# Performance work log

Measured on AMD Instinct MI355X. Metric: run time of the kernel, lower is better.

## Reference

```python
import jax, jax.numpy as jnp
import numpy as np

K_MASK = -2.3819763e+38
NUM_HEADS = 16
NUM_KV_HEADS = 8
HEAD_DIM = 128
FEATURES = 2048
QUERY_SCALE = 0.08838834764831845  # head_dim ** -0.5
ROPE_BASE = 10000
SOFT_CAP = 50.0
WINDOW = 1024


def apply_rope(inputs, positions, base_frequency=ROPE_BASE):
    # inputs: [B, L, N, H], positions: [B, L]
    head_dim = inputs.shape[-1]
    fraction = 2.0 * jnp.arange(0, head_dim // 2, dtype=jnp.float32) / head_dim
    timescale = jnp.asarray(base_frequency, jnp.float32) ** fraction
    sinusoid = positions[..., None].astype(jnp.float32) / timescale[None, None, :]
    sinusoid = sinusoid[..., None, :]  # [B, L, 1, H/2]
    sin, cos = jnp.sin(sinusoid), jnp.cos(sinusoid)
    first, second = jnp.split(inputs, 2, axis=-1)
    out = jnp.concatenate([first * cos - second * sin,
                           second * cos + first * sin], axis=-1)
    return out.astype(inputs.dtype)


def setup_inputs() -> dict:
    key = jax.random.key(0)
    ks = jax.random.split(key, 4)
    B, T, D = 2, 2048, FEATURES
    x = jax.random.normal(ks[0], (B, T, D), dtype=jnp.float32)
    segment_pos = jnp.broadcast_to(jnp.arange(T, dtype=jnp.int32)[None, :], (B, T))
    # causal prefill mask [B, T, S] with S == T
    attn_mask = jnp.broadcast_to(
        jnp.tril(jnp.ones((T, T), dtype=bool))[None], (B, T, T))
    wq = jax.random.normal(ks[1], (NUM_HEADS, D, HEAD_DIM), dtype=jnp.float32) * 0.02
    wkv = jax.random.normal(ks[2], (2, NUM_KV_HEADS, D, HEAD_DIM), dtype=jnp.float32) * 0.02
    wo = jax.random.normal(ks[3], (NUM_HEADS, HEAD_DIM, D), dtype=jnp.float32) * 0.02
    return {"x": x, "segment_pos": segment_pos, "attn_mask": attn_mask,
            "wq": wq, "wkv": wkv, "wo": wo}


def reference(x, segment_pos, attn_mask, wq, wkv, wo):
    # Projections
    q = jnp.einsum('BTD,NDH->BTNH', x, wq)              # [B,T,N,H]
    kv = jnp.einsum('BSD,CKDH->CBSKH', x, wkv)          # [2,B,S,K,H]
    k, v = kv[0], kv[1]

    # RoPE + query scaling
    q = apply_rope(q, segment_pos) * QUERY_SCALE
    k = apply_rope(k, segment_pos)

    # GQA: fold query heads into (K groups, G heads per group)
    B, T, N, H = q.shape
    K, G = NUM_KV_HEADS, N // NUM_KV_HEADS
    qg = q.reshape(B, T, K, G, H)
    logits = jnp.einsum('BTKGH,BSKH->BTKGS', qg, k).reshape(B, T, N, -1)

    # Logit soft-capping
    logits = jnp.tanh(logits / SOFT_CAP) * SOFT_CAP

    # Sliding-window mask (prefill: end_index=0, cache_len = S)
    S = attn_mask.shape[-1]
    cache_positions = jnp.arange(S)[None, None, :]       # [1,1,S]
    sp = segment_pos[:, :, None]                         # [B,T,1]
    sliding = (cache_positions > sp - WINDOW) & (cache_positions < sp + WINDOW)
    mask = jnp.logical_and(attn_mask, sliding)

    padded = jnp.where(mask[:, :, None, :], logits, K_MASK)
    probs = jax.nn.softmax(padded, axis=-1).astype(k.dtype)

    pg = probs.reshape(B, T, K, G, S)
    encoded = jnp.einsum('BTKGS,BSKH->BTKGH', pg, v).reshape(B, T, N, H)
    return jnp.einsum('BTNH,NHD->BTD', encoded, wo)
```

## Files before the change

kernel.cpp:

```cpp
#include <hip/hip_runtime.h>

typedef __attribute__((ext_vector_type(8))) short short8;
typedef __attribute__((ext_vector_type(4))) float f32x4;
typedef __attribute__((ext_vector_type(4))) float f4;
typedef __attribute__((ext_vector_type(4))) unsigned short u16x4;

__device__ __forceinline__ unsigned short f2bf(float f) {
    union { float f; unsigned int u; } v; v.f = f;
    unsigned int r = v.u + 0x7fffu + ((v.u >> 16) & 1u);
    return (unsigned short)(r >> 16);
}
__device__ __forceinline__ float bf2f(unsigned short h) {
    union { unsigned int u; float f; } v; v.u = ((unsigned int)h) << 16;
    return v.f;
}
__device__ __forceinline__ void gload_lds16(const void* g, void* l) {
    __builtin_amdgcn_global_load_lds(
        (const __attribute__((address_space(1))) unsigned int*)g,
        (__attribute__((address_space(3))) unsigned int*)l, 16, 0, 0);
}


__global__ void conv_x(const float* __restrict__ x, unsigned short* __restrict__ xb) {
    int i = blockIdx.x * 256 + threadIdx.x;
    f4 v = ((const f4*)x)[i];
    u16x4 o;
    o[0] = f2bf(v[0]); o[1] = f2bf(v[1]); o[2] = f2bf(v[2]); o[3] = f2bf(v[3]);
    ((u16x4*)xb)[i] = o;
}

__global__ void conv_wqkvt(const float* __restrict__ wq, const float* __restrict__ wkv,
                           unsigned short* __restrict__ wt) {
    __shared__ float tile[64 * 65];
    const int d0 = blockIdx.x * 64, f0 = blockIdx.y * 64;
    const int head = f0 >> 7;
    const int h0 = f0 & 127;
    const float* src;
    float scl;
    if (head < 16) { src = wq + (size_t)head * 2048 * 128; scl = 0.08838834764831845f; }
    else           { src = wkv + (size_t)(head - 16) * 2048 * 128; scl = 1.f; }
    {
        int hh = threadIdx.x & 63, dq = threadIdx.x >> 6;
        #pragma unroll
        for (int r = 0; r < 16; ++r) {
            int dd = r * 4 + dq;
            tile[dd * 65 + hh] = src[(size_t)(d0 + dd) * 128 + h0 + hh] * scl;
        }
    }
    __syncthreads();
    {
        int dd = threadIdx.x & 63, fq = threadIdx.x >> 6;
        #pragma unroll
        for (int r = 0; r < 16; ++r) {
            int fl = r * 4 + fq;
            wt[(size_t)(f0 + fl) * 2048 + d0 + dd] = f2bf(tile[dd * 65 + fl]);
        }
    }
}

__global__ void conv_wot(const float* __restrict__ wo, unsigned short* __restrict__ wt) {
    __shared__ float tile[64 * 65];
    const int d0 = blockIdx.x * 64, r0 = blockIdx.y * 64;
    int cc = threadIdx.x & 63, rq = threadIdx.x >> 6;
    #pragma unroll
    for (int r = 0; r < 16; ++r) {
        int rr = r * 4 + rq;
        tile[rr * 65 + cc] = wo[(size_t)(r0 + rr) * 2048 + d0 + cc];
    }
    __syncthreads();
    #pragma unroll
    for (int r = 0; r < 16; ++r) {
        int rr = r * 4 + rq;
        wt[(size_t)(d0 + rr) * 2048 + r0 + cc] = f2bf(tile[cc * 65 + rr]);
    }
}


__global__ __launch_bounds__(512, 2)
void gemm8p(const unsigned short* __restrict__ A,
            const unsigned short* __restrict__ Bt,
            unsigned short* __restrict__ C,
            int ldk, int ldc, int nt, int ksplit, size_t cstride) {
    __shared__ __align__(16) unsigned short LDS[65536];
    const int tid = threadIdx.x, lane = tid & 63, w = tid >> 6;
    const int wr = w >> 2, wc = w & 3;
    const int l15 = lane & 15, l4 = lane >> 4;
    int nwg = gridDim.x * gridDim.y;
    int wg = blockIdx.y * gridDim.x + blockIdx.x;
    int swz = (wg & 7) * (nwg >> 3) + (wg >> 3);
    int bx = swz % gridDim.x, by = swz / gridDim.x;
    int slice = 0;
    if (ksplit) { slice = by & 1; by >>= 1; }
    unsigned short* Cs = C + (size_t)slice * cstride;
    const int brow = by * 256, bcol = bx * 256;
    const size_t koff = (size_t)slice * nt * 64;
    const int wg_a = w & 3;
    const int wg_b = wr;
    const int rA = wg_a * 8 + (lane >> 3);
    const int rB = wg_b * 8 + (lane >> 3);
    const int cgS = ((lane & 7) ^ (lane >> 3)) * 8;
    const unsigned short* aP = A + (size_t)(brow + wr * 128 + rA) * ldk + koff + cgS;
    const unsigned short* bP = Bt + (size_t)(bcol + wc * 64 + rB) * ldk + koff + cgS;
    const int ldsA0 = wr * 8192 + (wg_a * 64 + lane) * 8;
    const int ldsB0 = wc * 4096 + (wg_b * 64 + lane) * 8;
    const int aRd = (wr * 128 + l15) * 64;
    const int bRd = (wc * 64 + l15) * 64;
    const int c0 = ((0 + l4) ^ (l15 & 7)) * 8;
    const int c1 = ((4 + l4) ^ (l15 & 7)) * 8;
    f32x4 acc[8][4] = {};
    gload_lds16(aP,                    &LDS[ldsA0]);
    gload_lds16(bP,                    &LDS[16384 + ldsB0]);
    gload_lds16(aP + (size_t)32 * ldk, &LDS[ldsA0 + 2048]);
    gload_lds16(bP + (size_t)16 * ldk, &LDS[16384 + ldsB0 + 1024]);
    gload_lds16(bP + (size_t)32 * ldk, &LDS[16384 + ldsB0 + 2048]);
    gload_lds16(bP + (size_t)48 * ldk, &LDS[16384 + ldsB0 + 3072]);
    gload_lds16(aP + (size_t)64 * ldk, &LDS[ldsA0 + 4096]);
    gload_lds16(aP + (size_t)96 * ldk, &LDS[ldsA0 + 6144]);
    asm volatile("s_waitcnt vmcnt(4)" ::: "memory");
    __builtin_amdgcn_s_barrier();
    __builtin_amdgcn_sched_barrier(0);

    short8 af[4][2], bl[2][2], bh[2][2];
    for (int t = 0; t < nt; ++t) {
        const int bufA = (t & 1) << 15, bufB = bufA + 16384;
        const bool pf = (t + 1) < nt;
        const int sA = ((t + 1) & 1) << 15, sB = sA + 16384;
        const unsigned short* ap = aP + (t + 1) * 64;
        const unsigned short* bp = bP + (t + 1) * 64;
        #pragma unroll
        for (int m = 0; m < 4; ++m) {
            af[m][0] = *(const short8*)&LDS[bufA + aRd + m * 1024 + c0];
            af[m][1] = *(const short8*)&LDS[bufA + aRd + m * 1024 + c1];
        }
        #pragma unroll
        for (int n = 0; n < 2; ++n) {
            bl[n][0] = *(const short8*)&LDS[bufB + bRd + n * 1024 + c0];
            bl[n][1] = *(const short8*)&LDS[bufB + bRd + n * 1024 + c1];
        }
        if (pf) { gload_lds16(ap, &LDS[sA + ldsA0]);
                  gload_lds16(bp, &LDS[sB + ldsB0]); }
        __builtin_amdgcn_s_barrier();
        __builtin_amdgcn_sched_barrier(0);
        __builtin_amdgcn_s_setprio(1);
        #pragma unroll
        for (int kk = 0; kk < 2; ++kk)
            #pragma unroll
            for (int m = 0; m < 4; ++m)
                #pragma unroll
                for (int n = 0; n < 2; ++n)
                    acc[m][n] = __builtin_amdgcn_mfma_f32_16x16x32_bf16(af[m][kk], bl[n][kk], acc[m][n], 0, 0, 0);
        __builtin_amdgcn_s_setprio(0);
        asm volatile("s_waitcnt vmcnt(4)" ::: "memory");
        __builtin_amdgcn_s_barrier();
        __builtin_amdgcn_sched_barrier(0);
        #pragma unroll
        for (int n = 0; n < 2; ++n) {
            bh[n][0] = *(const short8*)&LDS[bufB + bRd + (n + 2) * 1024 + c0];
            bh[n][1] = *(const short8*)&LDS[bufB + bRd + (n + 2) * 1024 + c1];
        }
        if (pf) { gload_lds16(ap + (size_t)32 * ldk, &LDS[sA + ldsA0 + 2048]);
                  gload_lds16(bp + (size_t)16 * ldk, &LDS[sB + ldsB0 + 1024]); }
        __builtin_amdgcn_s_barrier();
        __builtin_amdgcn_sched_barrier(0);
        __builtin_amdgcn_s_setprio(1);
        #pragma unroll
        for (int kk = 0; kk < 2; ++kk)
            #pragma unroll
            for (int m = 0; m < 4; ++m)
                #pragma unroll
                for (int n = 0; n < 2; ++n)
                    acc[m][n + 2] = __builtin_amdgcn_mfma_f32_16x16x32_bf16(af[m][kk], bh[n][kk], acc[m][n + 2], 0, 0, 0);
        __builtin_amdgcn_s_setprio(0);
        asm volatile("s_waitcnt vmcnt(4)" ::: "memory");
        __builtin_amdgcn_s_barrier();
        __builtin_amdgcn_sched_barrier(0);
        #pragma unroll
        for (int m = 0; m < 4; ++m) {
            af[m][0] = *(const short8*)&LDS[bufA + aRd + (m + 4) * 1024 + c0];
            af[m][1] = *(const short8*)&LDS[bufA + aRd + (m + 4) * 1024 + c1];
        }
        if (pf) { gload_lds16(bp + (size_t)32 * ldk, &LDS[sB + ldsB0 + 2048]);
                  gload_lds16(bp + (size_t)48 * ldk, &LDS[sB + ldsB0 + 3072]); }
        __builtin_amdgcn_s_barrier();
        __builtin_amdgcn_sched_barrier(0);
        __builtin_amdgcn_s_setprio(1);
        #pragma unroll
        for (int kk = 0; kk < 2; ++kk)
            #pragma unroll
            for (int m = 0; m < 4; ++m)
                #pragma unroll
                for (int n = 0; n < 2; ++n)
                    acc[m + 4][n] = __builtin_amdgcn_mfma_f32_16x16x32_bf16(af[m][kk], bl[n][kk], acc[m + 4][n], 0, 0, 0);
        __builtin_amdgcn_s_setprio(0);
        __builtin_amdgcn_s_barrier();
        __builtin_amdgcn_sched_barrier(0);
        if (pf) { gload_lds16(ap + (size_t)64 * ldk, &LDS[sA + ldsA0 + 4096]);
                  gload_lds16(ap + (size_t)96 * ldk, &LDS[sA + ldsA0 + 6144]); }
        __builtin_amdgcn_s_barrier();
        __builtin_amdgcn_sched_barrier(0);
        __builtin_amdgcn_s_setprio(1);
        #pragma unroll
        for (int kk = 0; kk < 2; ++kk)
            #pragma unroll
            for (int m = 0; m < 4; ++m)
                #pragma unroll
                for (int n = 0; n < 2; ++n)
                    acc[m + 4][n + 2] = __builtin_amdgcn_mfma_f32_16x16x32_bf16(af[m][kk], bh[n][kk], acc[m + 4][n + 2], 0, 0, 0);
        __builtin_amdgcn_s_setprio(0);
        asm volatile("s_waitcnt vmcnt(4)" ::: "memory");
        __builtin_amdgcn_s_barrier();
        __builtin_amdgcn_sched_barrier(0);
    }
    #pragma unroll
    for (int m = 0; m < 8; ++m)
        #pragma unroll
        for (int n = 0; n < 4; ++n)
            #pragma unroll
            for (int j = 0; j < 4; ++j) {
                int row = brow + wr * 128 + m * 16 + l4 * 4 + j;
                int col = bcol + wc * 64 + n * 16 + l15;
                Cs[(size_t)row * ldc + col] = f2bf(acc[m][n][j]);
            }
}

__global__ void addparts(const unsigned short* __restrict__ p0,
                         const unsigned short* __restrict__ p1,
                         float* __restrict__ out) {
    int i = blockIdx.x * 256 + threadIdx.x;
    short8 a = ((const short8*)p0)[i];
    short8 b = ((const short8*)p1)[i];
    f4 lo, hi;
    #pragma unroll
    for (int j = 0; j < 4; ++j)
        lo[j] = bf2f((unsigned short)a[j]) + bf2f((unsigned short)b[j]);
    #pragma unroll
    for (int j = 0; j < 4; ++j)
        hi[j] = bf2f((unsigned short)a[j + 4]) + bf2f((unsigned short)b[j + 4]);
    ((f4*)out)[2 * i] = lo;
    ((f4*)out)[2 * i + 1] = hi;
}

__global__ void rope_reshape(const unsigned short* __restrict__ qkv,
                             const int* __restrict__ segpos,
                             unsigned short* __restrict__ q_r,
                             unsigned short* __restrict__ k_r) {
    const int bt = blockIdx.x;
    const int hd = blockIdx.y * 2 + (threadIdx.x >> 7);
    const int b = bt >> 11, t = bt & 2047;
    const int h = threadIdx.x & 127;
    const unsigned short* in = (hd < 16)
        ? qkv + (size_t)bt * 4096 + hd * 128
        : qkv + (size_t)bt * 4096 + 2048 + (hd - 16) * 128;
    int pos = segpos[bt];
    int i = h & 63;
    float inv_ts = __expf((float)i * (-9.210340371976184f / 64.f));
    float ang = (float)pos * inv_ts;
    float s = __sinf(ang), c = __cosf(ang);
    float x1 = bf2f(in[i]);
    float x2 = bf2f(in[i + 64]);
    float o = (h < 64) ? (x1 * c - x2 * s) : (x2 * c + x1 * s);
    if (hd < 16) {
        q_r[((size_t)((b * 16 + hd) * 2048 + t)) * 128 + h] = f2bf(o);
    } else {
        int kh = hd - 16;
        k_r[((size_t)((b * 8 + kh) * 2048 + t)) * 128 + h] = f2bf(o);
    }
}

__global__ void v_transpose(const unsigned short* __restrict__ qkv,
                            unsigned short* __restrict__ v_t) {
    __shared__ unsigned short tile[64][72];
    const int tt0 = blockIdx.x * 64;
    const int kh = blockIdx.y >> 1, hb = (blockIdx.y & 1) * 64;
    const int b = blockIdx.z;
    int c = threadIdx.x & 63, rq = threadIdx.x >> 6;
    #pragma unroll
    for (int r = 0; r < 16; ++r) {
        int tt = r * 4 + rq;
        tile[tt][c] = qkv[(size_t)(b * 2048 + tt0 + tt) * 4096 + 3072 + kh * 128 + hb + c];
    }
    __syncthreads();
    #pragma unroll
    for (int r = 0; r < 16; ++r) {
        int hr = r * 4 + rq;
        v_t[((size_t)(b * 8 + kh) * 128 + hb + hr) * 2048 + tt0 + c] = tile[c][hr];
    }
}


__device__ __forceinline__ void stage_kv(const unsigned short* kbase, const unsigned short* vbase,
                                         unsigned short* Ksb, unsigned short* Vtb,
                                         int st, int tid) {
    #pragma unroll
    for (int r = 0; r < 2; ++r) {
        int e = (r * 512 + tid) * 8;
        int krow = e >> 7, kcol = e & 127;
        gload_lds16(kbase + (size_t)(st * 64 + krow) * 128 + (kcol ^ ((krow & 7) << 3)), Ksb + e);
        int vrow = e >> 6, vcol = e & 63;
        gload_lds16(vbase + (size_t)vrow * 2048 + st * 64 + (vcol ^ ((vrow & 7) << 3)), Vtb + e);
    }
}

__global__ __launch_bounds__(512, 4)
void attn_kernel(const unsigned short* __restrict__ q_r,
                 const unsigned short* __restrict__ k_r,
                 const unsigned short* __restrict__ v_t,
                 unsigned short* __restrict__ enc) {
    __shared__ __align__(16) unsigned short Ks[2][64 * 128];
    __shared__ __align__(16) unsigned short Vt[2][128 * 64];
    __shared__ __align__(16) unsigned short Pl[8][16 * 64];
    const int tid = threadIdx.x, lane = tid & 63, wave = tid >> 6;
    const int l15 = lane & 15, l4 = lane >> 4;
    const int flat = blockIdx.x;
    const int xcd = flat & 7, g = flat >> 3;
    const int pair = xcd * 2 + (g >> 5);
    const int qb = 31 - (g & 31);
    const int kh = pair >> 1, b = pair & 1;
    const int n = kh * 2 + (wave >> 2);
    const int wq = wave & 3;
    short8 qf[4];
    {
        const unsigned short* qp =
            q_r + ((size_t)((b * 16 + n) * 2048 + qb * 64 + wq * 16 + l15)) * 128 + l4 * 8;
        #pragma unroll
        for (int kk = 0; kk < 4; ++kk) qf[kk] = *(const short8*)(qp + kk * 32);
    }
    f32x4 Of[8] = {};
    float lrow[4] = {};
    int t_lo = qb * 64 - 1023; if (t_lo < 0) t_lo = 0;
    const int st0 = t_lo >> 6;
    const unsigned short* kbase = k_r + (size_t)(b * 8 + kh) * 2048 * 128;
    const unsigned short* vbase = v_t + (size_t)(b * 8 + kh) * 128 * 2048;

    stage_kv(kbase, vbase, Ks[0], Vt[0], st0, tid);
    __syncthreads();
    int cur = 0;
    for (int st = st0; st <= qb; ++st) {
        if (st < qb)
            stage_kv(kbase, vbase, Ks[cur ^ 1], Vt[cur ^ 1], st + 1, tid);
        f32x4 sf[4] = {};
        #pragma unroll
        for (int nc = 0; nc < 4; ++nc) {
            int row = nc * 16 + l15;
            int sw = (l15 & 7) << 3;
            #pragma unroll
            for (int kk = 0; kk < 4; ++kk) {
                short8 bfr = *(const short8*)&Ks[cur][row * 128 + ((kk * 32 + l4 * 8) ^ sw)];
                sf[nc] = __builtin_amdgcn_mfma_f32_16x16x32_bf16(qf[kk], bfr, sf[nc], 0, 0, 0);
            }
        }
        const int mode = (st == qb) ? 1 : ((qb >= 16 && st == st0) ? 2 : 0);
        #pragma unroll
        for (int j = 0; j < 4; ++j) {
            int trow = qb * 64 + wq * 16 + l4 * 4 + j;
            int prow = l4 * 4 + j;
            int psw = (prow & 7) << 3;
            #pragma unroll
            for (int nc = 0; nc < 4; ++nc) {
                float ex = __expf(sf[nc][j] * 0.04f);
                float p = __expf(-100.f * __builtin_amdgcn_rcpf(ex + 1.f));
                if (mode) {
                    int s = st * 64 + nc * 16 + l15;
                    bool ok = (mode == 1) ? (s <= trow) : (s >= trow - 1023);
                    p = ok ? p : 0.f;
                }
                lrow[j] += p;
                Pl[wave][prow * 64 + ((nc * 16 + l15) ^ psw)] = f2bf(p);
            }
        }
        {
            int asw = (l15 & 7) << 3;
            #pragma unroll
            for (int ks = 0; ks < 2; ++ks) {
                short8 af = *(const short8*)&Pl[wave][l15 * 64 + ((ks * 32 + l4 * 8) ^ asw)];
                #pragma unroll
                for (int hc = 0; hc < 8; ++hc) {
                    int vrow = hc * 16 + l15;
                    short8 bfr = *(const short8*)&Vt[cur][vrow * 64 + ((ks * 32 + l4 * 8) ^ asw)];
                    Of[hc] = __builtin_amdgcn_mfma_f32_16x16x32_bf16(af, bfr, Of[hc], 0, 0, 0);
                }
            }
        }
        __syncthreads();
        cur ^= 1;
    }
    float inv[4];
    #pragma unroll
    for (int j = 0; j < 4; ++j) {
        float l = lrow[j];
        l += __shfl_xor(l, 1); l += __shfl_xor(l, 2);
        l += __shfl_xor(l, 4); l += __shfl_xor(l, 8);
        inv[j] = 1.f / l;
    }
    #pragma unroll
    for (int hc = 0; hc < 8; ++hc)
        #pragma unroll
        for (int j = 0; j < 4; ++j) {
            size_t row = (size_t)(b * 2048 + qb * 64 + wq * 16 + l4 * 4 + j);
            enc[row * 2048 + n * 128 + hc * 16 + l15] = f2bf(Of[hc][j] * inv[j]);
        }
}


extern "C" void kernel_launch(void* const* d_in, const int* in_sizes, int n_in,
                              void* d_out, int out_size, void* d_ws, size_t ws_size,
                              hipStream_t stream) {
    const float* x   = (const float*)d_in[0];
    const int* segp  = (const int*)d_in[1];
    const float* wq  = (const float*)d_in[3];
    const float* wkv = (const float*)d_in[4];
    const float* wo  = (const float*)d_in[5];
    float* out = (float*)d_out;
    char* ws = (char*)d_ws;
    if (ws_size < ((size_t)96 << 20)) return;

    unsigned short* xb    = (unsigned short*)(ws);
    unsigned short* wqkvt = (unsigned short*)(ws + ((size_t)16 << 20));
    unsigned short* qkv   = (unsigned short*)(ws + ((size_t)32 << 20));
    unsigned short* q_r   = (unsigned short*)(ws + ((size_t)64 << 20));
    unsigned short* k_r   = (unsigned short*)(ws + ((size_t)80 << 20));
    unsigned short* v_t   = (unsigned short*)(ws + ((size_t)88 << 20));
    unsigned short* wo_t  = (unsigned short*)(ws + ((size_t)16 << 20));
    unsigned short* enc   = (unsigned short*)(ws + ((size_t)32 << 20));
    unsigned short* part  = (unsigned short*)(ws + ((size_t)64 << 20));

    conv_x<<<8192, 256, 0, stream>>>(x, xb);
    conv_wqkvt<<<dim3(32, 64), 256, 0, stream>>>(wq, wkv, wqkvt);
    gemm8p<<<dim3(16, 16), 512, 0, stream>>>(xb, wqkvt, qkv, 2048, 4096, 32, 0, 0);
    rope_reshape<<<dim3(4096, 12), 256, 0, stream>>>(qkv, segp, q_r, k_r);
    v_transpose<<<dim3(32, 16, 2), 256, 0, stream>>>(qkv, v_t);
    conv_wot<<<dim3(32, 32), 256, 0, stream>>>(wo, wo_t);
    attn_kernel<<<512, 512, 0, stream>>>(q_r, k_r, v_t, enc);
    gemm8p<<<dim3(8, 32), 512, 0, stream>>>(enc, wo_t, part, 2048, 2048, 16, 1, (size_t)4096 * 2048);
    addparts<<<4096, 256, 0, stream>>>(part, part + (size_t)4096 * 2048, out);
}
```

Baseline: 216.2 us.

## Restructure GEMM main loop with register double-buffering and simplify softmax exp path

The GEMM main loop becomes an unrolled pair of tiles. A and B fragments are double-buffered in registers, each full 64-wide K tile is prefetched two steps ahead with a single barrier per tile, and the two-step prefetch happens in the prologue. This cuts the four barriers and partial vmcnt waits per iteration down to one. In attention, the softcap and softmax exponentials are rewritten to use raw v_exp_f32, with the log2e factor folded into the K weight scale and the constant. P is packed to bf16 with v_cvt_pk_bf16_f32, and the MFMA sections are wrapped in setprio. The waits become full vmcnt(0) and lgkmcnt(0), which could expose load latency, and folding the scale into the K weights changes how the rounding falls.

```diff
diff --git a/kernel.cpp b/kernel.cpp
--- a/kernel.cpp
+++ b/kernel.cpp
@@ -5,6 +5,8 @@
 typedef __attribute__((ext_vector_type(4))) float f4;
 typedef __attribute__((ext_vector_type(4))) unsigned short u16x4;
 
+#define MFMA_B16 __builtin_amdgcn_mfma_f32_16x16x32_bf16
+
 __device__ __forceinline__ unsigned short f2bf(float f) {
     union { float f; unsigned int u; } v; v.f = f;
     unsigned int r = v.u + 0x7fffu + ((v.u >> 16) & 1u);
@@ -13,6 +15,14 @@
 __device__ __forceinline__ float bf2f(unsigned short h) {
     union { unsigned int u; float f; } v; v.u = ((unsigned int)h) << 16;
     return v.f;
+}
+__device__ __forceinline__ float fexp2(float x) {
+    float r; asm("v_exp_f32 %0, %1" : "=v"(r) : "v"(x)); return r;
+}
+__device__ __forceinline__ unsigned int cvt_pk_bf16(float lo, float hi) {
+    unsigned int r;
+    asm("v_cvt_pk_bf16_f32 %0, %1, %2" : "=v"(r) : "v"(lo), "v"(hi));
+    return r;
 }
 __device__ __forceinline__ void gload_lds16(const void* g, void* l) {
     __builtin_amdgcn_global_load_lds(
@@ -37,8 +47,9 @@
     const int h0 = f0 & 127;
     const float* src;
     float scl;
-    if (head < 16) { src = wq + (size_t)head * 2048 * 128; scl = 0.08838834764831845f; }
-    else           { src = wkv + (size_t)(head - 16) * 2048 * 128; scl = 1.f; }
+    if (head < 16)      { src = wq + (size_t)head * 2048 * 128;         scl = 0.08838834764831845f; }
+    else if (head < 24) { src = wkv + (size_t)(head - 16) * 2048 * 128; scl = 0.057707801635558534f; }
+    else                { src = wkv + (size_t)(head - 16) * 2048 * 128; scl = 1.f; }
     {
         int hh = threadIdx.x & 63, dq = threadIdx.x >> 6;
         #pragma unroll
@@ -75,6 +86,85 @@
     }
 }
 
+
+#define GTILE(T, BCL, BCH, BNL)                                                   \
+  {                                                                               \
+    const int bufA = ((T) & 1) << 15, bufB = bufA + 16384;                        \
+    const int nA = (((T) + 1) & 1) << 15, nB = nA + 16384;                        \
+    _Pragma("unroll")                                                             \
+    for (int n = 0; n < 2; ++n) {                                                 \
+      BCH[n][0] = *(const short8*)&LDS[bufB + bRd + (n + 2) * 1024 + c0];         \
+      BCH[n][1] = *(const short8*)&LDS[bufB + bRd + (n + 2) * 1024 + c1];         \
+    }                                                                             \
+    _Pragma("unroll")                                                             \
+    for (int m = 0; m < 4; ++m) {                                                 \
+      afh[m][0] = *(const short8*)&LDS[bufA + aRd + (m + 4) * 1024 + c0];         \
+      afh[m][1] = *(const short8*)&LDS[bufA + aRd + (m + 4) * 1024 + c1];         \
+    }                                                                             \
+    __builtin_amdgcn_sched_barrier(0);                                            \
+    __builtin_amdgcn_s_setprio(1);                                                \
+    _Pragma("unroll")                                                             \
+    for (int kk = 0; kk < 2; ++kk)                                                \
+      _Pragma("unroll")                                                           \
+      for (int m = 0; m < 4; ++m)                                                 \
+        _Pragma("unroll")                                                         \
+        for (int n = 0; n < 2; ++n)                                               \
+          acc[m][n] = MFMA_B16(afl[m][kk], BCL[n][kk], acc[m][n], 0, 0, 0);       \
+    _Pragma("unroll")                                                             \
+    for (int kk = 0; kk < 2; ++kk)                                                \
+      _Pragma("unroll")                                                           \
+      for (int m = 0; m < 4; ++m)                                                 \
+        _Pragma("unroll")                                                         \
+        for (int n = 0; n < 2; ++n)                                               \
+          acc[m][n + 2] = MFMA_B16(afl[m][kk], BCH[n][kk], acc[m][n + 2], 0, 0, 0);\
+    __builtin_amdgcn_s_setprio(0);                                                \
+    asm volatile("s_waitcnt vmcnt(0)" ::: "memory");                              \
+    asm volatile("s_waitcnt lgkmcnt(0)" ::: "memory");                            \
+    __builtin_amdgcn_sched_barrier(0);                                            \
+    __builtin_amdgcn_s_barrier();                                                 \
+    __builtin_amdgcn_sched_barrier(0);                                            \
+    if ((T) + 2 < nt) {                                                           \
+      const unsigned short* a2 = aP + (size_t)((T) + 2) * 64;                     \
+      const unsigned short* b2 = bP + (size_t)((T) + 2) * 64;                     \
+      gload_lds16(a2,                    &LDS[bufA + ldsA0]);                     \
+      gload_lds16(a2 + (size_t)32 * ldk, &LDS[bufA + ldsA0 + 2048]);              \
+      gload_lds16(a2 + (size_t)64 * ldk, &LDS[bufA + ldsA0 + 4096]);              \
+      gload_lds16(a2 + (size_t)96 * ldk, &LDS[bufA + ldsA0 + 6144]);              \
+      gload_lds16(b2,                    &LDS[bufB + ldsB0]);                     \
+      gload_lds16(b2 + (size_t)16 * ldk, &LDS[bufB + ldsB0 + 1024]);              \
+      gload_lds16(b2 + (size_t)32 * ldk, &LDS[bufB + ldsB0 + 2048]);              \
+      gload_lds16(b2 + (size_t)48 * ldk, &LDS[bufB + ldsB0 + 3072]);              \
+    }                                                                             \
+    if ((T) + 1 < nt) {                                                           \
+      _Pragma("unroll")                                                           \
+      for (int m = 0; m < 4; ++m) {                                               \
+        afl[m][0] = *(const short8*)&LDS[nA + aRd + m * 1024 + c0];               \
+        afl[m][1] = *(const short8*)&LDS[nA + aRd + m * 1024 + c1];               \
+      }                                                                           \
+      _Pragma("unroll")                                                           \
+      for (int n = 0; n < 2; ++n) {                                               \
+        BNL[n][0] = *(const short8*)&LDS[nB + bRd + n * 1024 + c0];               \
+        BNL[n][1] = *(const short8*)&LDS[nB + bRd + n * 1024 + c1];               \
+      }                                                                           \
+    }                                                                             \
+    __builtin_amdgcn_sched_barrier(0);                                            \
+    __builtin_amdgcn_s_setprio(1);                                                \
+    _Pragma("unroll")                                                             \
+    for (int kk = 0; kk < 2; ++kk)                                                \
+      _Pragma("unroll")                                                           \
+      for (int m = 0; m < 4; ++m)                                                 \
+        _Pragma("unroll")                                                         \
+        for (int n = 0; n < 2; ++n)                                               \
+          acc[m + 4][n] = MFMA_B16(afh[m][kk], BCL[n][kk], acc[m + 4][n], 0, 0, 0);\
+    _Pragma("unroll")                                                             \
+    for (int kk = 0; kk < 2; ++kk)                                                \
+      _Pragma("unroll")                                                           \
+      for (int m = 0; m < 4; ++m)                                                 \
+        _Pragma("unroll")                                                         \
+        for (int n = 0; n < 2; ++n)                                               \
+          acc[m + 4][n + 2] = MFMA_B16(afh[m][kk], BCH[n][kk], acc[m + 4][n + 2], 0, 0, 0);\
+    __builtin_amdgcn_s_setprio(0);                                                \
+  }
 
 __global__ __launch_bounds__(512, 2)
 void gemm8p(const unsigned short* __restrict__ A,
@@ -109,107 +199,45 @@
     const int c1 = ((4 + l4) ^ (l15 & 7)) * 8;
     f32x4 acc[8][4] = {};
     gload_lds16(aP,                    &LDS[ldsA0]);
+    gload_lds16(aP + (size_t)32 * ldk, &LDS[ldsA0 + 2048]);
+    gload_lds16(aP + (size_t)64 * ldk, &LDS[ldsA0 + 4096]);
+    gload_lds16(aP + (size_t)96 * ldk, &LDS[ldsA0 + 6144]);
     gload_lds16(bP,                    &LDS[16384 + ldsB0]);
-    gload_lds16(aP + (size_t)32 * ldk, &LDS[ldsA0 + 2048]);
     gload_lds16(bP + (size_t)16 * ldk, &LDS[16384 + ldsB0 + 1024]);
     gload_lds16(bP + (size_t)32 * ldk, &LDS[16384 + ldsB0 + 2048]);
     gload_lds16(bP + (size_t)48 * ldk, &LDS[16384 + ldsB0 + 3072]);
-    gload_lds16(aP + (size_t)64 * ldk, &LDS[ldsA0 + 4096]);
-    gload_lds16(aP + (size_t)96 * ldk, &LDS[ldsA0 + 6144]);
-    asm volatile("s_waitcnt vmcnt(4)" ::: "memory");
+    {
+        const unsigned short* a1 = aP + 64;
+        const unsigned short* b1 = bP + 64;
+        gload_lds16(a1,                    &LDS[32768 + ldsA0]);
+        gload_lds16(a1 + (size_t)32 * ldk, &LDS[32768 + ldsA0 + 2048]);
+        gload_lds16(a1 + (size_t)64 * ldk, &LDS[32768 + ldsA0 + 4096]);
+        gload_lds16(a1 + (size_t)96 * ldk, &LDS[32768 + ldsA0 + 6144]);
+        gload_lds16(b1,                    &LDS[49152 + ldsB0]);
+        gload_lds16(b1 + (size_t)16 * ldk, &LDS[49152 + ldsB0 + 1024]);
+        gload_lds16(b1 + (size_t)32 * ldk, &LDS[49152 + ldsB0 + 2048]);
+        gload_lds16(b1 + (size_t)48 * ldk, &LDS[49152 + ldsB0 + 3072]);
+    }
+    asm volatile("s_waitcnt vmcnt(8)" ::: "memory");
     __builtin_amdgcn_s_barrier();
     __builtin_amdgcn_sched_barrier(0);
 
-    short8 af[4][2], bl[2][2], bh[2][2];
-    for (int t = 0; t < nt; ++t) {
-        const int bufA = (t & 1) << 15, bufB = bufA + 16384;
-        const bool pf = (t + 1) < nt;
-        const int sA = ((t + 1) & 1) << 15, sB = sA + 16384;
-        const unsigned short* ap = aP + (t + 1) * 64;
-        const unsigned short* bp = bP + (t + 1) * 64;
-        #pragma unroll
-        for (int m = 0; m < 4; ++m) {
-            af[m][0] = *(const short8*)&LDS[bufA + aRd + m * 1024 + c0];
-            af[m][1] = *(const short8*)&LDS[bufA + aRd + m * 1024 + c1];
-        }
-        #pragma unroll
-        for (int n = 0; n < 2; ++n) {
-            bl[n][0] = *(const short8*)&LDS[bufB + bRd + n * 1024 + c0];
-            bl[n][1] = *(const short8*)&LDS[bufB + bRd + n * 1024 + c1];
-        }
-        if (pf) { gload_lds16(ap, &LDS[sA + ldsA0]);
-                  gload_lds16(bp, &LDS[sB + ldsB0]); }
-        __builtin_amdgcn_s_barrier();
-        __builtin_amdgcn_sched_barrier(0);
-        __builtin_amdgcn_s_setprio(1);
-        #pragma unroll
-        for (int kk = 0; kk < 2; ++kk)
-            #pragma unroll
-            for (int m = 0; m < 4; ++m)
-                #pragma unroll
-                for (int n = 0; n < 2; ++n)
-                    acc[m][n] = __builtin_amdgcn_mfma_f32_16x16x32_bf16(af[m][kk], bl[n][kk], acc[m][n], 0, 0, 0);
-        __builtin_amdgcn_s_setprio(0);
-        asm volatile("s_waitcnt vmcnt(4)" ::: "memory");
-        __builtin_amdgcn_s_barrier();
-        __builtin_amdgcn_sched_barrier(0);
-        #pragma unroll
-        for (int n = 0; n < 2; ++n) {
-            bh[n][0] = *(const short8*)&LDS[bufB + bRd + (n + 2) * 1024 + c0];
-            bh[n][1] = *(const short8*)&LDS[bufB + bRd + (n + 2) * 1024 + c1];
-        }
-        if (pf) { gload_lds16(ap + (size_t)32 * ldk, &LDS[sA + ldsA0 + 2048]);
-                  gload_lds16(bp + (size_t)16 * ldk, &LDS[sB + ldsB0 + 1024]); }
-        __builtin_amdgcn_s_barrier();
-        __builtin_amdgcn_sched_barrier(0);
-        __builtin_amdgcn_s_setprio(1);
-        #pragma unroll
-        for (int kk = 0; kk < 2; ++kk)
-            #pragma unroll
-            for (int m = 0; m < 4; ++m)
-                #pragma unroll
-                for (int n = 0; n < 2; ++n)
-                    acc[m][n + 2] = __builtin_amdgcn_mfma_f32_16x16x32_bf16(af[m][kk], bh[n][kk], acc[m][n + 2], 0, 0, 0);
-        __builtin_amdgcn_s_setprio(0);
-        asm volatile("s_waitcnt vmcnt(4)" ::: "memory");
-        __builtin_amdgcn_s_barrier();
-        __builtin_amdgcn_sched_barrier(0);
-        #pragma unroll
-        for (int m = 0; m < 4; ++m) {
-            af[m][0] = *(const short8*)&LDS[bufA + aRd + (m + 4) * 1024 + c0];
-            af[m][1] = *(const short8*)&LDS[bufA + aRd + (m + 4) * 1024 + c1];
-        }
-        if (pf) { gload_lds16(bp + (size_t)32 * ldk, &LDS[sB + ldsB0 + 2048]);
-                  gload_lds16(bp + (size_t)48 * ldk, &LDS[sB + ldsB0 + 3072]); }
-        __builtin_amdgcn_s_barrier();
-        __builtin_amdgcn_sched_barrier(0);
-        __builtin_amdgcn_s_setprio(1);
-        #pragma unroll
-        for (int kk = 0; kk < 2; ++kk)
-            #pragma unroll
-            for (int m = 0; m < 4; ++m)
-                #pragma unroll
-                for (int n = 0; n < 2; ++n)
-                    acc[m + 4][n] = __builtin_amdgcn_mfma_f32_16x16x32_bf16(af[m][kk], bl[n][kk], acc[m + 4][n], 0, 0, 0);
-        __builtin_amdgcn_s_setprio(0);
-        __builtin_amdgcn_s_barrier();
-        __builtin_amdgcn_sched_barrier(0);
-        if (pf) { gload_lds16(ap + (size_t)64 * ldk, &LDS[sA + ldsA0 + 4096]);
-                  gload_lds16(ap + (size_t)96 * ldk, &LDS[sA + ldsA0 + 6144]); }
-        __builtin_amdgcn_s_barrier();
-        __builtin_amdgcn_sched_barrier(0);
-        __builtin_amdgcn_s_setprio(1);
-        #pragma unroll
-        for (int kk = 0; kk < 2; ++kk)
-            #pragma unroll
-            for (int m = 0; m < 4; ++m)
-                #pragma unroll
-                for (int n = 0; n < 2; ++n)
-                    acc[m + 4][n + 2] = __builtin_amdgcn_mfma_f32_16x16x32_bf16(af[m][kk], bh[n][kk], acc[m + 4][n + 2], 0, 0, 0);
-        __builtin_amdgcn_s_setprio(0);
-        asm volatile("s_waitcnt vmcnt(4)" ::: "memory");
-        __builtin_amdgcn_s_barrier();
-        __builtin_amdgcn_sched_barrier(0);
+    short8 afl[4][2], afh[4][2], blA[2][2], bhA[2][2], blB[2][2], bhB[2][2];
+    #pragma unroll
+    for (int m = 0; m < 4; ++m) {
+        afl[m][0] = *(const short8*)&LDS[aRd + m * 1024 + c0];
+        afl[m][1] = *(const short8*)&LDS[aRd + m * 1024 + c1];
+    }
+    #pragma unroll
+    for (int n = 0; n < 2; ++n) {
+        blA[n][0] = *(const short8*)&LDS[16384 + bRd + n * 1024 + c0];
+        blA[n][1] = *(const short8*)&LDS[16384 + bRd + n * 1024 + c1];
+    }
+    __builtin_amdgcn_sched_barrier(0);
+
+    for (int t = 0; t < nt; t += 2) {
+        GTILE(t,     blA, bhA, blB);
+        GTILE(t + 1, blB, bhB, blA);
     }
     #pragma unroll
     for (int m = 0; m < 8; ++m)
@@ -339,6 +367,7 @@
         if (st < qb)
             stage_kv(kbase, vbase, Ks[cur ^ 1], Vt[cur ^ 1], st + 1, tid);
         f32x4 sf[4] = {};
+        __builtin_amdgcn_s_setprio(1);
         #pragma unroll
         for (int nc = 0; nc < 4; ++nc) {
             int row = nc * 16 + l15;
@@ -346,30 +375,40 @@
             #pragma unroll
             for (int kk = 0; kk < 4; ++kk) {
                 short8 bfr = *(const short8*)&Ks[cur][row * 128 + ((kk * 32 + l4 * 8) ^ sw)];
-                sf[nc] = __builtin_amdgcn_mfma_f32_16x16x32_bf16(qf[kk], bfr, sf[nc], 0, 0, 0);
+                sf[nc] = MFMA_B16(qf[kk], bfr, sf[nc], 0, 0, 0);
             }
         }
+        __builtin_amdgcn_s_setprio(0);
         const int mode = (st == qb) ? 1 : ((qb >= 16 && st == st0) ? 2 : 0);
         #pragma unroll
         for (int j = 0; j < 4; ++j) {
             int trow = qb * 64 + wq * 16 + l4 * 4 + j;
             int prow = l4 * 4 + j;
             int psw = (prow & 7) << 3;
+            float pp[4];
             #pragma unroll
             for (int nc = 0; nc < 4; ++nc) {
-                float ex = __expf(sf[nc][j] * 0.04f);
-                float p = __expf(-100.f * __builtin_amdgcn_rcpf(ex + 1.f));
+                float ex = fexp2(sf[nc][j]);
+                float p = fexp2(-144.26950408889634f * __builtin_amdgcn_rcpf(ex + 1.f));
                 if (mode) {
                     int s = st * 64 + nc * 16 + l15;
                     bool ok = (mode == 1) ? (s <= trow) : (s >= trow - 1023);
                     p = ok ? p : 0.f;
                 }
                 lrow[j] += p;
-                Pl[wave][prow * 64 + ((nc * 16 + l15) ^ psw)] = f2bf(p);
+                pp[nc] = p;
             }
+            unsigned int k01 = cvt_pk_bf16(pp[0], pp[1]);
+            unsigned int k23 = cvt_pk_bf16(pp[2], pp[3]);
+            unsigned short* Pr = &Pl[wave][prow * 64];
+            Pr[l15 ^ psw]        = (unsigned short)k01;
+            Pr[(16 + l15) ^ psw] = (unsigned short)(k01 >> 16);
+            Pr[(32 + l15) ^ psw] = (unsigned short)k23;
+            Pr[(48 + l15) ^ psw] = (unsigned short)(k23 >> 16);
         }
         {
             int asw = (l15 & 7) << 3;
+            __builtin_amdgcn_s_setprio(1);
             #pragma unroll
             for (int ks = 0; ks < 2; ++ks) {
                 short8 af = *(const short8*)&Pl[wave][l15 * 64 + ((ks * 32 + l4 * 8) ^ asw)];
@@ -377,9 +416,10 @@
                 for (int hc = 0; hc < 8; ++hc) {
                     int vrow = hc * 16 + l15;
                     short8 bfr = *(const short8*)&Vt[cur][vrow * 64 + ((ks * 32 + l4 * 8) ^ asw)];
-                    Of[hc] = __builtin_amdgcn_mfma_f32_16x16x32_bf16(af, bfr, Of[hc], 0, 0, 0);
+                    Of[hc] = MFMA_B16(af, bfr, Of[hc], 0, 0, 0);
                 }
             }
+            __builtin_amdgcn_s_setprio(0);
         }
         __syncthreads();
         cur ^= 1;
```

Result: slower. 572.6 us (+164.9%).
